# Kernel optimization log

Hardware: AMD Instinct MI355X
Metric: run time of the kernel (lower is better)

The kernel has to match this reference:

```python
import jax, jax.numpy as jnp
import numpy as np

DIMS, K_SIZE, V_SIZE = 256, 64, 64
B, T = 4, 4096


def setup_inputs() -> dict:
    key = jax.random.key(0)
    k1, k2, k3, k4 = jax.random.split(key, 4)
    # glorot-uniform-style init for the projection weights
    def glorot(k, fan_in, fan_out):
        lim = jnp.sqrt(6.0 / (fan_in + fan_out))
        return jax.random.uniform(k, (fan_in, fan_out), jnp.float32, -lim, lim)
    return {
        "inputs": jax.random.normal(k1, (B, T, DIMS), jnp.float32),
        "key_w": glorot(k2, DIMS, K_SIZE),
        "query_w": glorot(k3, DIMS, K_SIZE),
        "value_w": glorot(k4, DIMS, V_SIZE),
    }


def reference(inputs, key_w, query_w, value_w):
    # QKV projections: [B,T,D] @ [D,k] -> [B,T,k]
    keys = jnp.einsum('btd,dk->btk', inputs, key_w)
    queries = jnp.einsum('btd,dk->btk', inputs, query_w)
    values = jnp.einsum('btd,dv->btv', inputs, value_w)
    # full causal score matrix [B,T,T] (faithful to explicit triu mask)
    logits = jnp.einsum('bqk,bsk->bqs', queries, keys)
    q_idx = jnp.arange(logits.shape[1])[:, None]
    s_idx = jnp.arange(logits.shape[2])[None, :]
    causal = s_idx <= q_idx  # lower-triangular incl. diagonal
    sqrt_k = jnp.sqrt(jnp.asarray(key_w.shape[1], jnp.float32))
    masked = jnp.where(causal[None], logits, -jnp.inf)
    probs = jax.nn.softmax(masked / sqrt_k, axis=2)
    read = jnp.einsum('bqs,bsv->bqv', probs, values)
    return jnp.concatenate([inputs, read], axis=-1)  # [B,T,D+V]
```

## Files before the change

kernel.cpp:

```cpp
#include <hip/hip_runtime.h>

#define DIMS 256
#define HK 64
#define NB 4
#define NT 4096
#define BT (NB * NT)

typedef unsigned short u16;
typedef unsigned int u32;

using f32x4  = __attribute__((ext_vector_type(4))) float;
using bf16x8 = __attribute__((ext_vector_type(8))) short;

__device__ __forceinline__ u16 f2bf(float f) {
    u32 u = __float_as_uint(f);
    u = (u + 0x7FFFu + ((u >> 16) & 1u)) >> 16;
    return (u16)u;
}
__device__ __forceinline__ u32 pack2(float a, float b) {
    return (u32)f2bf(a) | ((u32)f2bf(b) << 16);
}
__device__ __forceinline__ bf16x8 cvt8(const float* p) {
    f32x4 a = *reinterpret_cast<const f32x4*>(p);
    f32x4 b = *reinterpret_cast<const f32x4*>(p + 4);
    union { u32 w[4]; bf16x8 v; } u;
    u.w[0] = pack2(a[0], a[1]); u.w[1] = pack2(a[2], a[3]);
    u.w[2] = pack2(b[0], b[1]); u.w[3] = pack2(b[2], b[3]);
    return u.v;
}

__global__ __launch_bounds__(256) void prep_kernel(
    const float* __restrict__ wk, const float* __restrict__ wq,
    const float* __restrict__ wv, u16* __restrict__ Wt)
{
    const int gid = (int)(blockIdx.x * 256 + threadIdx.x);
    const int e0 = gid * 4;
    const int m = e0 >> 14;
    const int r = e0 & 16383;
    const int col = r >> 8;
    const int k = r & 255;
    const float* w = (m == 0) ? wk : (m == 1) ? wq : wv;
    u32 w0 = pack2(w[(k + 0) * HK + col], w[(k + 1) * HK + col]);
    u32 w1 = pack2(w[(k + 2) * HK + col], w[(k + 3) * HK + col]);
    u32* p = reinterpret_cast<u32*>(Wt + e0);
    p[0] = w0; p[1] = w1;
}

__global__ __launch_bounds__(64) void proj_kernel(
    const float* __restrict__ x, const u16* __restrict__ Wt,
    u16* __restrict__ Qb, u16* __restrict__ Kb, u16* __restrict__ Vt)
{
    const int l = (int)threadIdx.x;
    const int lo = l & 15;
    const int g = l >> 4;
    const int bid = (int)blockIdx.x;
    const int m = bid % 3;
    const int q0 = (bid / 3) * 16;

    bf16x8 a[8];
    #pragma unroll
    for (int kf = 0; kf < 8; ++kf)
        a[kf] = cvt8(x + (size_t)(q0 + lo) * DIMS + kf * 32 + g * 8);

    const u16* wb = Wt + m * (HK * DIMS);
    f32x4 acc[4];
    #pragma unroll
    for (int c = 0; c < 4; ++c) acc[c] = f32x4{0.f, 0.f, 0.f, 0.f};

    #pragma unroll
    for (int c = 0; c < 4; ++c) {
        #pragma unroll
        for (int kf = 0; kf < 8; ++kf) {
            bf16x8 bf = *reinterpret_cast<const bf16x8*>(
                wb + (size_t)(16 * c + lo) * DIMS + kf * 32 + g * 8);
            acc[c] = __builtin_amdgcn_mfma_f32_16x16x32_bf16(a[kf], bf, acc[c], 0, 0, 0);
        }
    }

    if (m == 2) {
        #pragma unroll
        for (int c = 0; c < 4; ++c)
            #pragma unroll
            for (int ii = 0; ii < 4; ++ii) {
                const int grow = q0 + 4 * g + ii;
                Vt[(size_t)((grow >> 12) * HK + 16 * c + lo) * NT + (grow & (NT - 1))] =
                    f2bf(acc[c][ii]);
            }
    } else {
        const float sc = (m == 1) ? 0.125f * 1.44269504f : 1.0f;
        u16* dst = (m == 1) ? Qb : Kb;
        #pragma unroll
        for (int c = 0; c < 4; ++c)
            #pragma unroll
            for (int ii = 0; ii < 4; ++ii)
                dst[(size_t)(q0 + 4 * g + ii) * HK + 16 * c + lo] = f2bf(acc[c][ii] * sc);
    }
}

__global__ __launch_bounds__(64) void attn_kernel(
    const u16* __restrict__ Qb, const u16* __restrict__ Kb,
    const u16* __restrict__ Vt, float* __restrict__ Op, float* __restrict__ lp,
    const int S)
{
    __shared__ u16 Pl[32 * 40];
    const int l = (int)threadIdx.x;
    const int lo = l & 15;
    const int g = l >> 4;

    const int bid = (int)blockIdx.x;
    const int per = 4 * S;
    const int j = 127 - bid / per;
    const int r = bid % per;
    const int b = r / S;
    const int s = r % S;

    const int q0 = j * 32;
    const int nkv = j + 1;
    const int it0 = (s * nkv) / S;
    const int it1 = ((s + 1) * nkv) / S;

    bf16x8 qf[2][2];
    #pragma unroll
    for (int rh = 0; rh < 2; ++rh)
        #pragma unroll
        for (int kf = 0; kf < 2; ++kf)
            qf[rh][kf] = *reinterpret_cast<const bf16x8*>(
                Qb + (size_t)(b * NT + q0 + 16 * rh + lo) * HK + kf * 32 + g * 8);

    f32x4 o[2][4];
    float pls[2][4];
    #pragma unroll
    for (int rh = 0; rh < 2; ++rh)
        #pragma unroll
        for (int c = 0; c < 4; ++c) { o[rh][c] = f32x4{0.f, 0.f, 0.f, 0.f}; pls[rh][c] = 0.f; }

    for (int it = it0; it < it1; ++it) {
        const int s0 = it * 32;
        const bool domask = (it == nkv - 1);

        bf16x8 kfr[2][2];
        #pragma unroll
        for (int kh = 0; kh < 2; ++kh)
            #pragma unroll
            for (int kf = 0; kf < 2; ++kf)
                kfr[kh][kf] = *reinterpret_cast<const bf16x8*>(
                    Kb + (size_t)(b * NT + s0 + 16 * kh + lo) * HK + kf * 32 + g * 8);

        bf16x8 vf[4];
        #pragma unroll
        for (int c = 0; c < 4; ++c)
            vf[c] = *reinterpret_cast<const bf16x8*>(
                Vt + (size_t)(b * HK + 16 * c + lo) * NT + s0 + g * 8);

        const f32x4 zz = f32x4{0.f, 0.f, 0.f, 0.f};
        #pragma unroll
        for (int rh = 0; rh < 2; ++rh) {
            #pragma unroll
            for (int kh = 0; kh < 2; ++kh) {
                f32x4 sv = __builtin_amdgcn_mfma_f32_16x16x32_bf16(qf[rh][0], kfr[kh][0], zz, 0, 0, 0);
                sv = __builtin_amdgcn_mfma_f32_16x16x32_bf16(qf[rh][1], kfr[kh][1], sv, 0, 0, 0);
                #pragma unroll
                for (int ii = 0; ii < 4; ++ii) {
                    float v = sv[ii];
                    if (domask) {
                        if (s0 + 16 * kh + lo > q0 + 16 * rh + 4 * g + ii) v = -1e30f;
                    }
                    const float p = __builtin_amdgcn_exp2f(v - 28.0f);
                    pls[rh][ii] += p;
                    Pl[(16 * rh + 4 * g + ii) * 40 + 16 * kh + lo] = f2bf(p);
                }
            }
        }
        __syncthreads();
        bf16x8 pa[2];
        #pragma unroll
        for (int rh = 0; rh < 2; ++rh)
            pa[rh] = *reinterpret_cast<const bf16x8*>(&Pl[(16 * rh + lo) * 40 + g * 8]);
        #pragma unroll
        for (int rh = 0; rh < 2; ++rh)
            #pragma unroll
            for (int c = 0; c < 4; ++c)
                o[rh][c] = __builtin_amdgcn_mfma_f32_16x16x32_bf16(pa[rh], vf[c], o[rh][c], 0, 0, 0);
        __syncthreads();
    }

    const size_t rowbase = (size_t)s * BT + (size_t)b * NT + q0;
    #pragma unroll
    for (int rh = 0; rh < 2; ++rh) {
        #pragma unroll
        for (int c = 0; c < 4; ++c)
            #pragma unroll
            for (int ii = 0; ii < 4; ++ii)
                Op[(rowbase + 16 * rh + 4 * g + ii) * HK + 16 * c + lo] = o[rh][c][ii];
        #pragma unroll
        for (int ii = 0; ii < 4; ++ii) {
            float sum = pls[rh][ii];
            sum += __shfl_xor(sum, 1);
            sum += __shfl_xor(sum, 2);
            sum += __shfl_xor(sum, 4);
            sum += __shfl_xor(sum, 8);
            if (lo == 0) lp[rowbase + 16 * rh + 4 * g + ii] = sum;
        }
    }
}

__global__ __launch_bounds__(256) void merge_kernel(
    const float* __restrict__ x, const float* __restrict__ Op,
    const float* __restrict__ lp, float* __restrict__ out, const int S)
{
    const int stride = (int)(gridDim.x * blockDim.x);
    const int idx = (int)(blockIdx.x * blockDim.x + threadIdx.x);
    const f32x4* x4 = reinterpret_cast<const f32x4*>(x);
    const f32x4* Op4 = reinterpret_cast<const f32x4*>(Op);
    f32x4* out4 = reinterpret_cast<f32x4*>(out);

    for (int jj = idx; jj < BT * (DIMS / 4); jj += stride) {
        const int row = jj >> 6;
        const int c4 = jj & 63;
        out4[(size_t)row * 80 + c4] = x4[jj];
    }
    for (int jj = idx; jj < BT * 16; jj += stride) {
        const int row = jj >> 4;
        const int c4 = jj & 15;
        f32x4 acc = f32x4{0.f, 0.f, 0.f, 0.f};
        float li = 0.f;
        for (int ss = 0; ss < S; ++ss) {
            acc += Op4[((size_t)ss * BT + row) * 16 + c4];
            li += lp[(size_t)ss * BT + row];
        }
        const float inv = 1.0f / li;
        out4[(size_t)row * 80 + 64 + c4] = acc * inv;
    }
}

extern "C" void kernel_launch(void* const* d_in, const int* in_sizes, int n_in,
                              void* d_out, int out_size, void* d_ws, size_t ws_size,
                              hipStream_t stream) {
    (void)in_sizes; (void)n_in; (void)out_size;
    const float* x  = (const float*)d_in[0];
    const float* wk = (const float*)d_in[1];
    const float* wq = (const float*)d_in[2];
    const float* wv = (const float*)d_in[3];
    float* out = (float*)d_out;

    char* ws = (char*)d_ws;
    u16* Qb = (u16*)(ws);
    u16* Kb = (u16*)(ws + ((size_t)2 << 20));
    u16* Vt = (u16*)(ws + ((size_t)4 << 20));
    u16* Wt = (u16*)(ws + ((size_t)6 << 20));
    float* lp = (float*)(ws + ((size_t)6 << 20) + (256 << 10));
    float* Op = (float*)(ws + ((size_t)7 << 20));

    const size_t per_s = (size_t)BT * HK * 4;
    int S = 8;
    while (S > 1 && ((size_t)7 << 20) + (size_t)S * per_s > ws_size) S >>= 1;

    prep_kernel<<<48, 256, 0, stream>>>(wk, wq, wv, Wt);
    proj_kernel<<<3072, 64, 0, stream>>>(x, Wt, Qb, Kb, Vt);
    attn_kernel<<<128 * 4 * S, 64, 0, stream>>>(Qb, Kb, Vt, Op, lp, S);
    merge_kernel<<<2048, 256, 0, stream>>>(x, Op, lp, out, S);
}
```

Baseline: 80.09 us.

## Pre-convert inputs to bf16, unroll attention over two KV tiles, store bf16 partials

The prep kernel now copies x into the output and writes a bf16 copy of x, so the projection kernel loads bf16 directly instead of converting fp32 on the fly. Attention now handles two 32-wide KV tiles per step and specialises the masked diagonal tile with a template. It drops the per-iteration barriers, which is safe because each block is a single 64-thread wave. It also raises wave priority around the MFMA sections. Split-K partial outputs are stored as bf16 to halve workspace traffic, and the merge kernel becomes a simple one-row-slice-per-thread reduction; this costs some precision in the partial sums.

```diff
diff --git a/kernel.cpp b/kernel.cpp
--- a/kernel.cpp
+++ b/kernel.cpp
@@ -5,12 +5,14 @@
 #define NB 4
 #define NT 4096
 #define BT (NB * NT)
+#define SMAX 8
 
 typedef unsigned short u16;
 typedef unsigned int u32;
 
 using f32x4  = __attribute__((ext_vector_type(4))) float;
 using bf16x8 = __attribute__((ext_vector_type(8))) short;
+using u32x2  = __attribute__((ext_vector_type(2))) u32;
 
 __device__ __forceinline__ u16 f2bf(float f) {
     u32 u = __float_as_uint(f);
@@ -20,34 +22,48 @@
 __device__ __forceinline__ u32 pack2(float a, float b) {
     return (u32)f2bf(a) | ((u32)f2bf(b) << 16);
 }
-__device__ __forceinline__ bf16x8 cvt8(const float* p) {
-    f32x4 a = *reinterpret_cast<const f32x4*>(p);
-    f32x4 b = *reinterpret_cast<const f32x4*>(p + 4);
-    union { u32 w[4]; bf16x8 v; } u;
-    u.w[0] = pack2(a[0], a[1]); u.w[1] = pack2(a[2], a[3]);
-    u.w[2] = pack2(b[0], b[1]); u.w[3] = pack2(b[2], b[3]);
-    return u.v;
+__device__ __forceinline__ float bf2f(short h) {
+    return __uint_as_float(((u32)(u16)h) << 16);
+}
+__device__ __forceinline__ bf16x8 ldb8(const u16* p) {
+    return *reinterpret_cast<const bf16x8*>(p);
 }
 
 __global__ __launch_bounds__(256) void prep_kernel(
-    const float* __restrict__ wk, const float* __restrict__ wq,
-    const float* __restrict__ wv, u16* __restrict__ Wt)
-{
-    const int gid = (int)(blockIdx.x * 256 + threadIdx.x);
-    const int e0 = gid * 4;
-    const int m = e0 >> 14;
-    const int r = e0 & 16383;
-    const int col = r >> 8;
-    const int k = r & 255;
-    const float* w = (m == 0) ? wk : (m == 1) ? wq : wv;
-    u32 w0 = pack2(w[(k + 0) * HK + col], w[(k + 1) * HK + col]);
-    u32 w1 = pack2(w[(k + 2) * HK + col], w[(k + 3) * HK + col]);
-    u32* p = reinterpret_cast<u32*>(Wt + e0);
-    p[0] = w0; p[1] = w1;
+    const float* __restrict__ x, const float* __restrict__ wk,
+    const float* __restrict__ wq, const float* __restrict__ wv,
+    float* __restrict__ out, u32* __restrict__ xb2, u16* __restrict__ Wt)
+{
+    const int stride = (int)(gridDim.x * blockDim.x);
+    const int idx = (int)(blockIdx.x * blockDim.x + threadIdx.x);
+    const f32x4* x4 = reinterpret_cast<const f32x4*>(x);
+    f32x4* out4 = reinterpret_cast<f32x4*>(out);
+    u32x2* xbv = reinterpret_cast<u32x2*>(xb2);
+
+    for (int i = idx; i < BT * 64; i += stride) {
+        f32x4 v = x4[i];
+        out4[(size_t)(i >> 6) * 80 + (i & 63)] = v;
+        u32x2 w;
+        w.x = pack2(v[0], v[1]);
+        w.y = pack2(v[2], v[3]);
+        xbv[i] = w;
+    }
+    for (int i = idx; i < 12288; i += stride) {
+        const int e0 = i * 4;
+        const int m = e0 >> 14;
+        const int r = e0 & 16383;
+        const int col = r >> 8;
+        const int k = r & 255;
+        const float* w = (m == 0) ? wk : (m == 1) ? wq : wv;
+        u32 w0 = pack2(w[(k + 0) * HK + col], w[(k + 1) * HK + col]);
+        u32 w1 = pack2(w[(k + 2) * HK + col], w[(k + 3) * HK + col]);
+        u32* p = reinterpret_cast<u32*>(Wt + e0);
+        p[0] = w0; p[1] = w1;
+    }
 }
 
 __global__ __launch_bounds__(64) void proj_kernel(
-    const float* __restrict__ x, const u16* __restrict__ Wt,
+    const u16* __restrict__ xb, const u16* __restrict__ Wt,
     u16* __restrict__ Qb, u16* __restrict__ Kb, u16* __restrict__ Vt)
 {
     const int l = (int)threadIdx.x;
@@ -58,24 +74,25 @@
     const int q0 = (bid / 3) * 16;
 
     bf16x8 a[8];
-    #pragma unroll
-    for (int kf = 0; kf < 8; ++kf)
-        a[kf] = cvt8(x + (size_t)(q0 + lo) * DIMS + kf * 32 + g * 8);
+    const u16* xrow = xb + (size_t)(q0 + lo) * DIMS + g * 8;
+    #pragma unroll
+    for (int kf = 0; kf < 8; ++kf) a[kf] = ldb8(xrow + kf * 32);
 
     const u16* wb = Wt + m * (HK * DIMS);
     f32x4 acc[4];
     #pragma unroll
     for (int c = 0; c < 4; ++c) acc[c] = f32x4{0.f, 0.f, 0.f, 0.f};
 
+    __builtin_amdgcn_s_setprio(1);
     #pragma unroll
     for (int c = 0; c < 4; ++c) {
         #pragma unroll
         for (int kf = 0; kf < 8; ++kf) {
-            bf16x8 bf = *reinterpret_cast<const bf16x8*>(
-                wb + (size_t)(16 * c + lo) * DIMS + kf * 32 + g * 8);
+            bf16x8 bf = ldb8(wb + (size_t)(16 * c + lo) * DIMS + kf * 32 + g * 8);
             acc[c] = __builtin_amdgcn_mfma_f32_16x16x32_bf16(a[kf], bf, acc[c], 0, 0, 0);
         }
     }
+    __builtin_amdgcn_s_setprio(0);
 
     if (m == 2) {
         #pragma unroll
@@ -97,12 +114,87 @@
     }
 }
 
+template<bool MASK>
+__device__ __forceinline__ void qk_tile(
+    const u16* __restrict__ Kb_b, int s0, int colbase,
+    const bf16x8 (&qf)[2][2], float (&pls)[2][4],
+    u16 (&Pl)[32 * 72], int lo, int g, int q0)
+{
+    bf16x8 kk[2][2];
+    #pragma unroll
+    for (int kh = 0; kh < 2; ++kh)
+        #pragma unroll
+        for (int kf = 0; kf < 2; ++kf)
+            kk[kh][kf] = ldb8(Kb_b + (size_t)(s0 + 16 * kh + lo) * HK + kf * 32 + g * 8);
+
+    const f32x4 zz = f32x4{0.f, 0.f, 0.f, 0.f};
+    f32x4 sv[2][2];
+    __builtin_amdgcn_s_setprio(1);
+    #pragma unroll
+    for (int rh = 0; rh < 2; ++rh)
+        #pragma unroll
+        for (int kh = 0; kh < 2; ++kh) {
+            sv[rh][kh] = __builtin_amdgcn_mfma_f32_16x16x32_bf16(qf[rh][0], kk[kh][0], zz, 0, 0, 0);
+            sv[rh][kh] = __builtin_amdgcn_mfma_f32_16x16x32_bf16(qf[rh][1], kk[kh][1], sv[rh][kh], 0, 0, 0);
+        }
+    __builtin_amdgcn_s_setprio(0);
+
+    #pragma unroll
+    for (int rh = 0; rh < 2; ++rh)
+        #pragma unroll
+        for (int kh = 0; kh < 2; ++kh)
+            #pragma unroll
+            for (int ii = 0; ii < 4; ++ii) {
+                float v = sv[rh][kh][ii];
+                if (MASK) {
+                    if (s0 + 16 * kh + lo > q0 + 16 * rh + 4 * g + ii) v = -1e30f;
+                }
+                const float p = __builtin_amdgcn_exp2f(v - 28.0f);
+                pls[rh][ii] += p;
+                Pl[(16 * rh + 4 * g + ii) * 72 + colbase + 16 * kh + lo] = f2bf(p);
+            }
+}
+
+template<int NKF, bool MASK>
+__device__ __forceinline__ void body(
+    const u16* __restrict__ Kb_b, const u16* __restrict__ Vb, int s0,
+    const bf16x8 (&qf)[2][2], float (&pls)[2][4], f32x4 (&o)[2][4],
+    u16 (&Pl)[32 * 72], int lo, int g, int q0)
+{
+    bf16x8 vf[NKF][4];
+    #pragma unroll
+    for (int kf = 0; kf < NKF; ++kf)
+        #pragma unroll
+        for (int c = 0; c < 4; ++c)
+            vf[kf][c] = ldb8(Vb + (size_t)(16 * c + lo) * NT + s0 + kf * 32 + g * 8);
+
+    qk_tile<MASK>(Kb_b, s0, 0, qf, pls, Pl, lo, g, q0);
+    if (NKF == 2) qk_tile<false>(Kb_b, s0 + 32, 32, qf, pls, Pl, lo, g, q0);
+
+    bf16x8 pa[2][NKF];
+    #pragma unroll
+    for (int rh = 0; rh < 2; ++rh)
+        #pragma unroll
+        for (int kf = 0; kf < NKF; ++kf)
+            pa[rh][kf] = *reinterpret_cast<const bf16x8*>(&Pl[(16 * rh + lo) * 72 + kf * 32 + g * 8]);
+
+    __builtin_amdgcn_s_setprio(1);
+    #pragma unroll
+    for (int rh = 0; rh < 2; ++rh)
+        #pragma unroll
+        for (int c = 0; c < 4; ++c)
+            #pragma unroll
+            for (int kf = 0; kf < NKF; ++kf)
+                o[rh][c] = __builtin_amdgcn_mfma_f32_16x16x32_bf16(pa[rh][kf], vf[kf][c], o[rh][c], 0, 0, 0);
+    __builtin_amdgcn_s_setprio(0);
+}
+
 __global__ __launch_bounds__(64) void attn_kernel(
     const u16* __restrict__ Qb, const u16* __restrict__ Kb,
-    const u16* __restrict__ Vt, float* __restrict__ Op, float* __restrict__ lp,
+    const u16* __restrict__ Vt, u16* __restrict__ Opb, float* __restrict__ lp,
     const int S)
 {
-    __shared__ u16 Pl[32 * 40];
+    __shared__ u16 Pl[32 * 72];
     const int l = (int)threadIdx.x;
     const int lo = l & 15;
     const int g = l >> 4;
@@ -119,13 +211,15 @@
     const int it0 = (s * nkv) / S;
     const int it1 = ((s + 1) * nkv) / S;
 
+    const u16* Kb_b = Kb + (size_t)b * NT * HK;
+    const u16* Vb = Vt + (size_t)b * HK * NT;
+
     bf16x8 qf[2][2];
     #pragma unroll
     for (int rh = 0; rh < 2; ++rh)
         #pragma unroll
         for (int kf = 0; kf < 2; ++kf)
-            qf[rh][kf] = *reinterpret_cast<const bf16x8*>(
-                Qb + (size_t)(b * NT + q0 + 16 * rh + lo) * HK + kf * 32 + g * 8);
+            qf[rh][kf] = ldb8(Qb + (size_t)(b * NT + q0 + 16 * rh + lo) * HK + kf * 32 + g * 8);
 
     f32x4 o[2][4];
     float pls[2][4];
@@ -134,55 +228,14 @@
         #pragma unroll
         for (int c = 0; c < 4; ++c) { o[rh][c] = f32x4{0.f, 0.f, 0.f, 0.f}; pls[rh][c] = 0.f; }
 
-    for (int it = it0; it < it1; ++it) {
-        const int s0 = it * 32;
-        const bool domask = (it == nkv - 1);
-
-        bf16x8 kfr[2][2];
-        #pragma unroll
-        for (int kh = 0; kh < 2; ++kh)
-            #pragma unroll
-            for (int kf = 0; kf < 2; ++kf)
-                kfr[kh][kf] = *reinterpret_cast<const bf16x8*>(
-                    Kb + (size_t)(b * NT + s0 + 16 * kh + lo) * HK + kf * 32 + g * 8);
-
-        bf16x8 vf[4];
-        #pragma unroll
-        for (int c = 0; c < 4; ++c)
-            vf[c] = *reinterpret_cast<const bf16x8*>(
-                Vt + (size_t)(b * HK + 16 * c + lo) * NT + s0 + g * 8);
-
-        const f32x4 zz = f32x4{0.f, 0.f, 0.f, 0.f};
-        #pragma unroll
-        for (int rh = 0; rh < 2; ++rh) {
-            #pragma unroll
-            for (int kh = 0; kh < 2; ++kh) {
-                f32x4 sv = __builtin_amdgcn_mfma_f32_16x16x32_bf16(qf[rh][0], kfr[kh][0], zz, 0, 0, 0);
-                sv = __builtin_amdgcn_mfma_f32_16x16x32_bf16(qf[rh][1], kfr[kh][1], sv, 0, 0, 0);
-                #pragma unroll
-                for (int ii = 0; ii < 4; ++ii) {
-                    float v = sv[ii];
-                    if (domask) {
-                        if (s0 + 16 * kh + lo > q0 + 16 * rh + 4 * g + ii) v = -1e30f;
-                    }
-                    const float p = __builtin_amdgcn_exp2f(v - 28.0f);
-                    pls[rh][ii] += p;
-                    Pl[(16 * rh + 4 * g + ii) * 40 + 16 * kh + lo] = f2bf(p);
-                }
-            }
-        }
-        __syncthreads();
-        bf16x8 pa[2];
-        #pragma unroll
-        for (int rh = 0; rh < 2; ++rh)
-            pa[rh] = *reinterpret_cast<const bf16x8*>(&Pl[(16 * rh + lo) * 40 + g * 8]);
-        #pragma unroll
-        for (int rh = 0; rh < 2; ++rh)
-            #pragma unroll
-            for (int c = 0; c < 4; ++c)
-                o[rh][c] = __builtin_amdgcn_mfma_f32_16x16x32_bf16(pa[rh], vf[c], o[rh][c], 0, 0, 0);
-        __syncthreads();
-    }
+    int it = it0;
+    const int itE = (s == S - 1) ? it1 - 1 : it1;
+    for (; it + 1 < itE; it += 2)
+        body<2, false>(Kb_b, Vb, it * 32, qf, pls, o, Pl, lo, g, q0);
+    if (it < itE)
+        body<1, false>(Kb_b, Vb, it * 32, qf, pls, o, Pl, lo, g, q0);
+    if (s == S - 1)
+        body<1, true>(Kb_b, Vb, (nkv - 1) * 32, qf, pls, o, Pl, lo, g, q0);
 
     const size_t rowbase = (size_t)s * BT + (size_t)b * NT + q0;
     #pragma unroll
@@ -191,7 +244,7 @@
         for (int c = 0; c < 4; ++c)
             #pragma unroll
             for (int ii = 0; ii < 4; ++ii)
-                Op[(rowbase + 16 * rh + 4 * g + ii) * HK + 16 * c + lo] = o[rh][c][ii];
+                Opb[(rowbase + 16 * rh + 4 * g + ii) * HK + 16 * c + lo] = f2bf(o[rh][c][ii]);
         #pragma unroll
         for (int ii = 0; ii < 4; ++ii) {
             float sum = pls[rh][ii];
@@ -205,32 +258,30 @@
 }
 
 __global__ __launch_bounds__(256) void merge_kernel(
-    const float* __restrict__ x, const float* __restrict__ Op,
-    const float* __restrict__ lp, float* __restrict__ out, const int S)
-{
-    const int stride = (int)(gridDim.x * blockDim.x);
-    const int idx = (int)(blockIdx.x * blockDim.x + threadIdx.x);
-    const f32x4* x4 = reinterpret_cast<const f32x4*>(x);
-    const f32x4* Op4 = reinterpret_cast<const f32x4*>(Op);
-    f32x4* out4 = reinterpret_cast<f32x4*>(out);
-
-    for (int jj = idx; jj < BT * (DIMS / 4); jj += stride) {
-        const int row = jj >> 6;
-        const int c4 = jj & 63;
-        out4[(size_t)row * 80 + c4] = x4[jj];
-    }
-    for (int jj = idx; jj < BT * 16; jj += stride) {
-        const int row = jj >> 4;
-        const int c4 = jj & 15;
-        f32x4 acc = f32x4{0.f, 0.f, 0.f, 0.f};
-        float li = 0.f;
-        for (int ss = 0; ss < S; ++ss) {
-            acc += Op4[((size_t)ss * BT + row) * 16 + c4];
-            li += lp[(size_t)ss * BT + row];
-        }
-        const float inv = 1.0f / li;
-        out4[(size_t)row * 80 + 64 + c4] = acc * inv;
-    }
+    const u16* __restrict__ Opb, const float* __restrict__ lp,
+    float* __restrict__ out, const int S)
+{
+    const int idx = (int)(blockIdx.x * 256 + threadIdx.x);
+    const int row = idx >> 3;
+    const int c8 = (idx & 7) * 8;
+
+    float li = 0.f;
+    for (int s = 0; s < S; ++s) li += lp[(size_t)s * BT + row];
+
+    float acc[8];
+    #pragma unroll
+    for (int k = 0; k < 8; ++k) acc[k] = 0.f;
+    for (int s = 0; s < S; ++s) {
+        bf16x8 v = ldb8(Opb + ((size_t)s * BT + row) * HK + c8);
+        #pragma unroll
+        for (int k = 0; k < 8; ++k) acc[k] += bf2f(v[k]);
+    }
+    const float inv = 1.0f / li;
+    f32x4 r0 = f32x4{acc[0] * inv, acc[1] * inv, acc[2] * inv, acc[3] * inv};
+    f32x4 r1 = f32x4{acc[4] * inv, acc[5] * inv, acc[6] * inv, acc[7] * inv};
+    f32x4* dst = reinterpret_cast<f32x4*>(out + (size_t)row * 320 + 256 + c8);
+    dst[0] = r0;
+    dst[1] = r1;
 }
 
 extern "C" void kernel_launch(void* const* d_in, const int* in_sizes, int n_in,
@@ -244,19 +295,20 @@
     float* out = (float*)d_out;
 
     char* ws = (char*)d_ws;
-    u16* Qb = (u16*)(ws);
-    u16* Kb = (u16*)(ws + ((size_t)2 << 20));
-    u16* Vt = (u16*)(ws + ((size_t)4 << 20));
-    u16* Wt = (u16*)(ws + ((size_t)6 << 20));
-    float* lp = (float*)(ws + ((size_t)6 << 20) + (256 << 10));
-    float* Op = (float*)(ws + ((size_t)7 << 20));
-
-    const size_t per_s = (size_t)BT * HK * 4;
-    int S = 8;
-    while (S > 1 && ((size_t)7 << 20) + (size_t)S * per_s > ws_size) S >>= 1;
-
-    prep_kernel<<<48, 256, 0, stream>>>(wk, wq, wv, Wt);
-    proj_kernel<<<3072, 64, 0, stream>>>(x, Wt, Qb, Kb, Vt);
-    attn_kernel<<<128 * 4 * S, 64, 0, stream>>>(Qb, Kb, Vt, Op, lp, S);
-    merge_kernel<<<2048, 256, 0, stream>>>(x, Op, lp, out, S);
-}
+    u16* Qb  = (u16*)(ws);
+    u16* Kb  = (u16*)(ws + ((size_t)2  << 20));
+    u16* Vt  = (u16*)(ws + ((size_t)4  << 20));
+    u32* xb2 = (u32*)(ws + ((size_t)6  << 20));
+    u16* xb  = (u16*)xb2;
+    u16* Wt  = (u16*)(ws + ((size_t)14 << 20));
+    float* lp = (float*)(ws + ((size_t)15 << 20));
+    u16* Opb = (u16*)(ws + ((size_t)16 << 20));
+
+    int S = SMAX;
+    while (S > 1 && ((size_t)16 << 20) + (size_t)S * BT * HK * 2 > ws_size) S >>= 1;
+
+    prep_kernel<<<1024, 256, 0, stream>>>(x, wk, wq, wv, out, xb2, Wt);
+    proj_kernel<<<3072, 64, 0, stream>>>(xb, Wt, Qb, Kb, Vt);
+    attn_kernel<<<128 * 4 * S, 64, 0, stream>>>(Qb, Kb, Vt, Opb, lp, S);
+    merge_kernel<<<512, 256, 0, stream>>>(Opb, lp, out, S);
+}
```

Result: faster. 75.09 us (-6.2%).
